# Kernel optimization log

Measured on AMD Instinct MI355X. Metric: run time of the kernel, lower is better.

Reference implementation:

```python
import jax, jax.numpy as jnp
import numpy as np

DIM = 512
NUM_HEADS = 16
HEAD_DIM = DIM // NUM_HEADS  # 32
SCALE = HEAD_DIM ** -0.5
B_, N = 1024, 49  # num_windows*batch, window_size**2


def setup_inputs() -> dict:
    key = jax.random.key(0)
    ks = jax.random.split(key, 12)
    s = DIM ** -0.5
    return {
        "x": jax.random.normal(ks[0], (B_, N, DIM), jnp.float32),
        "x2": jax.random.normal(ks[1], (B_, N, DIM), jnp.float32),
        "x3": jax.random.normal(ks[2], (B_, N, DIM), jnp.float32),
        # Linear weights stored as [in, out] (y = x @ W + b), same math as torch Linear
        "Wqkv": jax.random.normal(ks[3], (DIM, 3 * DIM), jnp.float32) * s,
        "bqkv": jnp.zeros((3 * DIM,), jnp.float32),
        "Wqkv2": jax.random.normal(ks[4], (DIM, 3 * DIM), jnp.float32) * s,
        "bqkv2": jnp.zeros((3 * DIM,), jnp.float32),
        "Wgw": jax.random.normal(ks[5], (DIM, DIM), jnp.float32) * s,
        "bgw": jnp.zeros((DIM,), jnp.float32),
        "Wproj": jax.random.normal(ks[6], (DIM, DIM), jnp.float32) * s,
        "bproj": jnp.zeros((DIM,), jnp.float32),
        "a": jnp.zeros((1,), jnp.float32),
    }


def reference(x, x2, x3, Wqkv, bqkv, Wqkv2, bqkv2, Wgw, bgw, Wproj, bproj, a):
    B, Nn, C = x.shape
    H, D = NUM_HEADS, HEAD_DIM
    # qkv from x: only k is actually used downstream
    qkv = (x @ Wqkv + bqkv).reshape(B, Nn, 3, H, D)
    k = jnp.transpose(qkv[:, :, 1], (0, 2, 1, 3))  # [B,H,N,D]
    # qkv2 from x3: q1 (gated query) and v1 (value + residual)
    qkv1 = (x3 @ Wqkv2 + bqkv2).reshape(B, Nn, 3, H, D)
    q1 = jnp.transpose(qkv1[:, :, 0], (0, 2, 1, 3))  # [B,H,N,D]
    v1 = jnp.transpose(qkv1[:, :, 2], (0, 2, 1, 3))  # [B,H,N,D]
    # gate from x2
    gw = jnp.transpose((x2 @ Wgw + bgw).reshape(B, Nn, H, D), (0, 2, 1, 3))
    q = q1 * SCALE * gw
    attn = jax.nn.softmax(jnp.einsum("bhnd,bhmd->bhnm", q, k), axis=-1)
    out = jnp.einsum("bhnm,bhmd->bhnd", attn, v1) + v1 * a
    out = jnp.transpose(out, (0, 2, 1, 3)).reshape(B, Nn, C)
    return out @ Wproj + bproj
```

## Files before the change

kernel.cpp:

```cpp
#include <hip/hip_runtime.h>

#define MR 50176
#define DIMC 512
#define NWIN 49
#define NBATCH 1024
#define NHEADS 16
#define ATTN_SCALE 0.17677669529663689f

typedef short bf16x8 __attribute__((ext_vector_type(8)));
typedef float f32x4 __attribute__((ext_vector_type(4)));
typedef unsigned int u32;

__device__ __forceinline__ unsigned short f2bf(float f) {
  union { float f; u32 u; } v; v.f = f;
  u32 u = v.u;
  u += 0x7FFFu + ((u >> 16) & 1u);
  return (unsigned short)(u >> 16);
}
__device__ __forceinline__ float bits_f(u32 u) {
  union { u32 u; float f; } v; v.u = u; return v.f;
}

__device__ __forceinline__ size_t pk_chunk(int r, int c) {
  return (((size_t)(r >> 3) * 8 + (c >> 3)) * 64 +
          ((r & 7) * 8 + ((c & 7) ^ (r & 7)))) << 4;
}

typedef const __attribute__((address_space(1))) u32* gp_t;
typedef __attribute__((address_space(3))) u32* lp_t;
__device__ __forceinline__ void glds16(const void* g, void* l) {
  __builtin_amdgcn_global_load_lds((gp_t)g, (lp_t)l, 16, 0, 0);
}

__global__ __launch_bounds__(256) void conv_pack3(
    const float* __restrict__ X0, const float* __restrict__ X1,
    const float* __restrict__ X2, short* __restrict__ P0,
    short* __restrict__ P1, short* __restrict__ P2) {
  const float* X = (blockIdx.y == 0) ? X0 : (blockIdx.y == 1) ? X1 : X2;
  short* Xp = (blockIdx.y == 0) ? P0 : (blockIdx.y == 1) ? P1 : P2;
  const int tid = blockIdx.x * 256 + threadIdx.x;
  const int li = tid & 63, gl = tid >> 6;
  const int kline = gl & 7, group = gl >> 3;
  const int rr = li >> 3, pp = li & 7;
  const int row = group * 8 + rr;
  const int k = kline * 64 + ((pp ^ rr) << 3);
  const float* src = X + (size_t)row * DIMC + k;
  const float4 a = *(const float4*)src;
  const float4 b = *(const float4*)(src + 4);
  u32 w0 = (u32)f2bf(a.x) | ((u32)f2bf(a.y) << 16);
  u32 w1 = (u32)f2bf(a.z) | ((u32)f2bf(a.w) << 16);
  u32 w2 = (u32)f2bf(b.x) | ((u32)f2bf(b.y) << 16);
  u32 w3 = (u32)f2bf(b.z) | ((u32)f2bf(b.w) << 16);
  ((uint4*)Xp)[tid] = make_uint4(w0, w1, w2, w3);
}

__global__ __launch_bounds__(256) void prep_w_pack(
    const float* __restrict__ Wqkv, const float* __restrict__ Wqkv2,
    const float* __restrict__ Wgw, const float* __restrict__ Wproj,
    short* __restrict__ Wp) {
  const int tid = blockIdx.x * 256 + threadIdx.x;
  const int li = tid & 63, gl = tid >> 6;
  const int kline = gl & 7, group = gl >> 3;
  const int rr = li >> 3, pp = li & 7;
  const int row = group * 8 + rr;
  const int k = kline * 64 + ((pp ^ rr) << 3);
  const int n = row & 511, mat = row >> 9;
  const float* W; int ldw, col;
  if (mat == 0)      { W = Wqkv;  ldw = 1536; col = 512 + n; }
  else if (mat == 1) { W = Wqkv2; ldw = 1536; col = n; }
  else if (mat == 2) { W = Wqkv2; ldw = 1536; col = 1024 + n; }
  else if (mat == 3) { W = Wgw;   ldw = 512;  col = n; }
  else               { W = Wproj; ldw = 512;  col = n; }
  unsigned short h[8];
#pragma unroll
  for (int j = 0; j < 8; ++j) h[j] = f2bf(W[(size_t)(k + j) * ldw + col]);
  u32 w0 = (u32)h[0] | ((u32)h[1] << 16);
  u32 w1 = (u32)h[2] | ((u32)h[3] << 16);
  u32 w2 = (u32)h[4] | ((u32)h[5] << 16);
  u32 w3 = (u32)h[6] | ((u32)h[7] << 16);
  ((uint4*)Wp)[tid] = make_uint4(w0, w1, w2, w3);
}

struct GemmCfg {
  const short* A[4];
  const float* bias[4];
  short* out[4];
  int wrow0[4];
};

template <int LNX, bool OUT_F32>
__global__ __launch_bounds__(256) void gemm_glds(
    GemmCfg cfg, const short* __restrict__ Wp, float* __restrict__ outf) {
  __shared__ short As[128 * 64];
  __shared__ short Bs[128 * 64];

  const int t = threadIdx.x, w = t >> 6, lane = t & 63;
  const int l15 = lane & 15, q = lane >> 4;
  const int wm = w >> 1, wn = w & 1;
  const int id = blockIdx.x;
  const int xcd = id & 7, slot = id >> 3;
  const int bx = slot & ((1 << LNX) - 1);
  const int y = xcd + ((slot >> LNX) << 3);
  const int row0 = y * 128;
  const int unit = bx >> 2, sub = bx & 3;
  const short* Ap = cfg.A[unit];
  const float* bias = cfg.bias[unit];
  short* outb = cfg.out[unit];
  const int nw0 = cfg.wrow0[unit] + sub * 128;
  const int col0 = sub * 128;

  f32x4 acc[4][4];
#pragma unroll
  for (int i = 0; i < 4; ++i)
#pragma unroll
    for (int j = 0; j < 4; ++j) acc[i][j] = {0.f, 0.f, 0.f, 0.f};

  const size_t lb = (size_t)lane * 16;
  const int r7 = l15 & 7, hi8 = l15 >> 3;

  for (int kt = 0; kt < 8; ++kt) {
    __syncthreads();
#pragma unroll
    for (int jj = 0; jj < 4; ++jj) {
      const int rg = w * 4 + jj;
      const char* ga = (const char*)Ap + ((((size_t)(row0 >> 3) + rg) * 8 + kt) << 10);
      glds16(ga + lb, &As[(size_t)rg << 9]);
      const char* gb = (const char*)Wp + ((((size_t)(nw0 >> 3) + rg) * 8 + kt) << 10);
      glds16(gb + lb, &Bs[(size_t)rg << 9]);
    }
    __syncthreads();
#pragma unroll
    for (int s = 0; s < 2; ++s) {
      const int sw = ((s * 4 + q) ^ r7);
      const int pos = (r7 * 8 + sw) * 8;
      bf16x8 af[4], bfr[4];
#pragma unroll
      for (int i = 0; i < 4; ++i)
        af[i] = *(const bf16x8*)&As[((wm * 8 + i * 2 + hi8) << 9) + pos];
#pragma unroll
      for (int j = 0; j < 4; ++j)
        bfr[j] = *(const bf16x8*)&Bs[((wn * 8 + j * 2 + hi8) << 9) + pos];
#pragma unroll
      for (int i = 0; i < 4; ++i)
#pragma unroll
        for (int j = 0; j < 4; ++j)
          acc[i][j] = __builtin_amdgcn_mfma_f32_16x16x32_bf16(af[i], bfr[j],
                                                              acc[i][j], 0, 0, 0);
    }
  }

#pragma unroll
  for (int j = 0; j < 4; ++j) {
    const int C = col0 + wn * 64 + j * 16 + l15;
    const float bv = bias[C];
#pragma unroll
    for (int i = 0; i < 4; ++i) {
#pragma unroll
      for (int r = 0; r < 4; ++r) {
        const int R = row0 + wm * 64 + i * 16 + q * 4 + r;
        const float val = acc[i][j][r] + bv;
        if constexpr (OUT_F32)
          outf[(size_t)R * DIMC + C] = val;
        else
          *(short*)((char*)outb + pk_chunk(R, C >> 3) + ((C & 7) << 1)) =
              (short)f2bf(val);
      }
    }
  }
}

__global__ __launch_bounds__(256) void attn_mfma(
    const short* __restrict__ kbuf, const short* __restrict__ qbuf,
    const short* __restrict__ vbuf, const short* __restrict__ gbuf,
    const float* __restrict__ a_scalar, short* __restrict__ obuf) {
  __shared__ short pls[4][64 * 40];
  __shared__ short vls[4][32 * 72];

  const int t = threadIdx.x;
  const int w = t >> 6, lane = t & 63;
  const int l15 = lane & 15, q = lane >> 4;
  const int wid = blockIdx.x * 4 + w;
  const int b = wid >> 4, h = wid & 15;
  const int row0 = b * NWIN;
  const float aval = a_scalar[0];
  short* P = pls[w];
  short* VT = vls[w];

#pragma unroll
  for (int it = 0; it < 5; ++it) {
    int off = (it * 64 + lane) * 8;
    if (off < 32 * 72) *(uint4*)&VT[off] = make_uint4(0u, 0u, 0u, 0u);
  }

  bf16x8 kf[4];
#pragma unroll
  for (int mj = 0; mj < 4; ++mj) {
    int m = mj * 16 + l15; if (m > 48) m = 48;
    kf[mj] = *(const bf16x8*)((const char*)kbuf + pk_chunk(row0 + m, h * 4 + q));
  }
  bf16x8 qf[4];
#pragma unroll
  for (int mi = 0; mi < 4; ++mi) {
    int n = mi * 16 + l15; if (n > 48) n = 48;
    const size_t off = pk_chunk(row0 + n, h * 4 + q);
    uint4 qa = *(const uint4*)((const char*)qbuf + off);
    uint4 ga = *(const uint4*)((const char*)gbuf + off);
    u32* qa_ = (u32*)&qa;
    u32* ga_ = (u32*)&ga;
    uint4 res; u32* r_ = (u32*)&res;
#pragma unroll
    for (int jj = 0; jj < 4; ++jj) {
      float lo = bits_f(qa_[jj] << 16) * bits_f(ga_[jj] << 16);
      float hi = bits_f(qa_[jj] & 0xffff0000u) * bits_f(ga_[jj] & 0xffff0000u);
      r_[jj] = (u32)f2bf(lo) | ((u32)f2bf(hi) << 16);
    }
    qf[mi] = *(bf16x8*)&res;
  }
#pragma unroll
  for (int it = 0; it < 4; ++it) {
    int chunk = it * 64 + lane;
    if (chunk < 196) {
      int n = chunk >> 2, dcq = chunk & 3;
      uint4 v = *(const uint4*)((const char*)vbuf + pk_chunk(row0 + n, h * 4 + dcq));
      const short* vs = (const short*)&v;
#pragma unroll
      for (int j = 0; j < 8; ++j) VT[(dcq * 8 + j) * 72 + n] = vs[j];
    }
  }

  f32x4 s[4][4];
#pragma unroll
  for (int mi = 0; mi < 4; ++mi)
#pragma unroll
    for (int nj = 0; nj < 4; ++nj) {
      f32x4 z = {0.f, 0.f, 0.f, 0.f};
      s[mi][nj] = __builtin_amdgcn_mfma_f32_16x16x32_bf16(qf[mi], kf[nj], z, 0, 0, 0);
    }

#pragma unroll
  for (int mi = 0; mi < 4; ++mi)
#pragma unroll
    for (int nj = 0; nj < 4; ++nj) {
      const bool valid = (nj * 16 + l15) < NWIN;
#pragma unroll
      for (int r = 0; r < 4; ++r)
        s[mi][nj][r] = valid ? __expf(ATTN_SCALE * s[mi][nj][r]) : 0.f;
    }

  float lsum[4][4];
#pragma unroll
  for (int mi = 0; mi < 4; ++mi)
#pragma unroll
    for (int r = 0; r < 4; ++r) {
      float part = s[mi][0][r] + s[mi][1][r] + s[mi][2][r] + s[mi][3][r];
      part += __shfl_xor(part, 1, 64);
      part += __shfl_xor(part, 2, 64);
      part += __shfl_xor(part, 4, 64);
      part += __shfl_xor(part, 8, 64);
      lsum[mi][r] = part;
    }

  f32x4 o[4][2];
#pragma unroll
  for (int mi = 0; mi < 4; ++mi)
#pragma unroll
    for (int dj = 0; dj < 2; ++dj) o[mi][dj] = {0.f, 0.f, 0.f, 0.f};

#pragma unroll
  for (int c = 0; c < 2; ++c) {
#pragma unroll
    for (int mi = 0; mi < 4; ++mi)
#pragma unroll
      for (int njh = 0; njh < 2; ++njh) {
        const int nj = c * 2 + njh;
        const int m = nj * 16 + l15;
#pragma unroll
        for (int r = 0; r < 4; ++r) {
          const int n = mi * 16 + q * 4 + r;
          float val = s[mi][nj][r];
          if (m == n) val += aval * lsum[mi][r];
          P[n * 40 + njh * 16 + l15] = (short)f2bf(val);
        }
      }
    bf16x8 bfr[2];
#pragma unroll
    for (int dj = 0; dj < 2; ++dj)
      bfr[dj] = *(const bf16x8*)&VT[(dj * 16 + l15) * 72 + c * 32 + q * 8];
#pragma unroll
    for (int mi = 0; mi < 4; ++mi) {
      bf16x8 af = *(const bf16x8*)&P[(mi * 16 + l15) * 40 + q * 8];
#pragma unroll
      for (int dj = 0; dj < 2; ++dj)
        o[mi][dj] = __builtin_amdgcn_mfma_f32_16x16x32_bf16(af, bfr[dj],
                                                            o[mi][dj], 0, 0, 0);
    }
  }

#pragma unroll
  for (int mi = 0; mi < 4; ++mi)
#pragma unroll
    for (int r = 0; r < 4; ++r) {
      const int n = mi * 16 + q * 4 + r;
      if (n < NWIN) {
        const float rl = 1.0f / lsum[mi][r];
#pragma unroll
        for (int dj = 0; dj < 2; ++dj) {
          const int d = dj * 16 + l15;
          *(short*)((char*)obuf + pk_chunk(row0 + n, h * 4 + (d >> 3)) +
                    ((d & 7) << 1)) = (short)f2bf(o[mi][dj][r] * rl);
        }
      }
    }
}

extern "C" void kernel_launch(void* const* d_in, const int* in_sizes, int n_in,
                              void* d_out, int out_size, void* d_ws,
                              size_t ws_size, hipStream_t stream) {
  const float* x     = (const float*)d_in[0];
  const float* x2    = (const float*)d_in[1];
  const float* x3    = (const float*)d_in[2];
  const float* Wqkv  = (const float*)d_in[3];
  const float* bqkv  = (const float*)d_in[4];
  const float* Wqkv2 = (const float*)d_in[5];
  const float* bqkv2 = (const float*)d_in[6];
  const float* Wgw   = (const float*)d_in[7];
  const float* bgw   = (const float*)d_in[8];
  const float* Wproj = (const float*)d_in[9];
  const float* bproj = (const float*)d_in[10];
  const float* a     = (const float*)d_in[11];

  char* ws = (char*)d_ws;
  const size_t WTSZ = (size_t)2560 * DIMC * sizeof(short);
  const size_t BSZ  = (size_t)MR * DIMC * sizeof(short);
  short* wt_all = (short*)ws;

  prep_w_pack<<<640, 256, 0, stream>>>(Wqkv, Wqkv2, Wgw, Wproj, wt_all);

  const int convg = MR * DIMC / 8 / 256;

  if (ws_size >= WTSZ + 7 * BSZ) {
    short* xp   = (short*)(ws + WTSZ);
    short* x2p  = (short*)(ws + WTSZ + BSZ);
    short* x3p  = (short*)(ws + WTSZ + 2 * BSZ);
    short* kbuf = (short*)(ws + WTSZ + 3 * BSZ);
    short* qbuf = (short*)(ws + WTSZ + 4 * BSZ);
    short* vbuf = (short*)(ws + WTSZ + 5 * BSZ);
    short* gbuf = (short*)(ws + WTSZ + 6 * BSZ);
    short* obuf = xp;

    conv_pack3<<<dim3(convg, 3), 256, 0, stream>>>(x, x2, x3, xp, x2p, x3p);

    GemmCfg s1;
    s1.A[0] = xp;  s1.A[1] = x3p; s1.A[2] = x3p; s1.A[3] = x2p;
    s1.bias[0] = bqkv + 512; s1.bias[1] = bqkv2;
    s1.bias[2] = bqkv2 + 1024; s1.bias[3] = bgw;
    s1.out[0] = kbuf; s1.out[1] = qbuf; s1.out[2] = vbuf; s1.out[3] = gbuf;
    s1.wrow0[0] = 0; s1.wrow0[1] = 512; s1.wrow0[2] = 1024; s1.wrow0[3] = 1536;
    gemm_glds<4, false><<<16 * 392, 256, 0, stream>>>(s1, wt_all, nullptr);

    attn_mfma<<<(NBATCH * NHEADS) / 4, 256, 0, stream>>>(kbuf, qbuf, vbuf,
                                                         gbuf, a, obuf);

    GemmCfg pj = {};
    pj.A[0] = obuf; pj.bias[0] = bproj; pj.out[0] = nullptr; pj.wrow0[0] = 2048;
    gemm_glds<2, true><<<4 * 392, 256, 0, stream>>>(pj, wt_all, (float*)d_out);
  } else {
    short* cb   = (short*)(ws + WTSZ);
    short* kbuf = (short*)(ws + WTSZ + BSZ);
    short* qbuf = (short*)(ws + WTSZ + 2 * BSZ);
    short* vbuf = (short*)(ws + WTSZ + 3 * BSZ);
    short* gbuf = (short*)(ws + WTSZ + 4 * BSZ);
    short* obuf = cb;

    conv_pack3<<<dim3(convg, 1), 256, 0, stream>>>(x, x, x, cb, cb, cb);
    GemmCfg ck = {};
    ck.A[0] = cb; ck.bias[0] = bqkv + 512; ck.out[0] = kbuf; ck.wrow0[0] = 0;
    gemm_glds<2, false><<<4 * 392, 256, 0, stream>>>(ck, wt_all, nullptr);

    conv_pack3<<<dim3(convg, 1), 256, 0, stream>>>(x3, x3, x3, cb, cb, cb);
    GemmCfg cqv = {};
    cqv.A[0] = cb; cqv.A[1] = cb;
    cqv.bias[0] = bqkv2; cqv.bias[1] = bqkv2 + 1024;
    cqv.out[0] = qbuf; cqv.out[1] = vbuf;
    cqv.wrow0[0] = 512; cqv.wrow0[1] = 1024;
    gemm_glds<3, false><<<8 * 392, 256, 0, stream>>>(cqv, wt_all, nullptr);

    conv_pack3<<<dim3(convg, 1), 256, 0, stream>>>(x2, x2, x2, cb, cb, cb);
    GemmCfg cg = {};
    cg.A[0] = cb; cg.bias[0] = bgw; cg.out[0] = gbuf; cg.wrow0[0] = 1536;
    gemm_glds<2, false><<<4 * 392, 256, 0, stream>>>(cg, wt_all, nullptr);

    attn_mfma<<<(NBATCH * NHEADS) / 4, 256, 0, stream>>>(kbuf, qbuf, vbuf,
                                                         gbuf, a, obuf);

    GemmCfg pj = {};
    pj.A[0] = obuf; pj.bias[0] = bproj; pj.wrow0[0] = 2048;
    gemm_glds<2, true><<<4 * 392, 256, 0, stream>>>(pj, wt_all, (float*)d_out);
  }
}
```

Before: 624.4 us.

## Replace GEMM with 256x256-tile, 8-wave, double-buffered pipelined kernel

```diff
diff --git a/kernel.cpp b/kernel.cpp
--- a/kernel.cpp
+++ b/kernel.cpp
@@ -88,81 +88,175 @@
   int wrow0[4];
 };
 
-template <int LNX, bool OUT_F32>
-__global__ __launch_bounds__(256) void gemm_glds(
+template <int LBX, bool OUT_F32>
+__global__ __launch_bounds__(512, 2) void gemm8p(
     GemmCfg cfg, const short* __restrict__ Wp, float* __restrict__ outf) {
-  __shared__ short As[128 * 64];
-  __shared__ short Bs[128 * 64];
+  __shared__ short As[2][16384];
+  __shared__ short Bs[2][16384];
 
   const int t = threadIdx.x, w = t >> 6, lane = t & 63;
   const int l15 = lane & 15, q = lane >> 4;
-  const int wm = w >> 1, wn = w & 1;
+  const int wm = w >> 2, wn = w & 3;
+  const int r7 = l15 & 7, hi8 = l15 >> 3;
+
   const int id = blockIdx.x;
-  const int xcd = id & 7, slot = id >> 3;
-  const int bx = slot & ((1 << LNX) - 1);
-  const int y = xcd + ((slot >> LNX) << 3);
-  const int row0 = y * 128;
-  const int unit = bx >> 2, sub = bx & 3;
+  const int spx = gridDim.x >> 3;
+  const int flat = (id & 7) * spx + (id >> 3);
+  const int bx = flat & ((1 << LBX) - 1);
+  const int mtile = flat >> LBX;
+  const int unit = bx >> 1, sub = bx & 1;
+  const int row0 = mtile * 256;
+  const int col0 = sub * 256;
   const short* Ap = cfg.A[unit];
   const float* bias = cfg.bias[unit];
   short* outb = cfg.out[unit];
-  const int nw0 = cfg.wrow0[unit] + sub * 128;
-  const int col0 = sub * 128;
-
-  f32x4 acc[4][4];
-#pragma unroll
-  for (int i = 0; i < 4; ++i)
+  const int nw0 = cfg.wrow0[unit] + sub * 256;
+
+  const int in0 = (r7 * 8 + (q ^ r7)) << 4;
+  const int in1 = (r7 * 8 + ((4 + q) ^ r7)) << 4;
+
+  auto stage = [&](int pt, int c) {
+    if (c >= 8) return;
+    const int slot = c & 1;
+#pragma unroll
+    for (int jj = 0; jj < 2; ++jj) {
+      const int cb = w * 2 + jj;
+      if (pt < 2) {
+        const int rowblk = ((cb & 8) ? 16 : 0) + pt * 8 + (cb & 7);
+        const char* ga = (const char*)Ap +
+            ((((size_t)(row0 >> 3) + rowblk) * 8 + c) << 10) +
+            (size_t)lane * 16;
+        glds16(ga, (char*)&As[slot][0] + (((pt << 4) + cb) << 10));
+      } else {
+        const int p = pt - 2;
+        const int colblk = ((cb >> 2) << 3) + p * 4 + (cb & 3);
+        const char* gb = (const char*)Wp +
+            ((((size_t)(nw0 >> 3) + colblk) * 8 + c) << 10) +
+            (size_t)lane * 16;
+        glds16(gb, (char*)&Bs[slot][0] + (((p << 4) + cb) << 10));
+      }
+    }
+  };
+
+  f32x4 acc[8][4];
+#pragma unroll
+  for (int i = 0; i < 8; ++i)
 #pragma unroll
     for (int j = 0; j < 4; ++j) acc[i][j] = {0.f, 0.f, 0.f, 0.f};
 
-  const size_t lb = (size_t)lane * 16;
-  const int r7 = l15 & 7, hi8 = l15 >> 3;
-
-  for (int kt = 0; kt < 8; ++kt) {
-    __syncthreads();
-#pragma unroll
-    for (int jj = 0; jj < 4; ++jj) {
-      const int rg = w * 4 + jj;
-      const char* ga = (const char*)Ap + ((((size_t)(row0 >> 3) + rg) * 8 + kt) << 10);
-      glds16(ga + lb, &As[(size_t)rg << 9]);
-      const char* gb = (const char*)Wp + ((((size_t)(nw0 >> 3) + rg) * 8 + kt) << 10);
-      glds16(gb + lb, &Bs[(size_t)rg << 9]);
-    }
-    __syncthreads();
-#pragma unroll
-    for (int s = 0; s < 2; ++s) {
-      const int sw = ((s * 4 + q) ^ r7);
-      const int pos = (r7 * 8 + sw) * 8;
-      bf16x8 af[4], bfr[4];
-#pragma unroll
-      for (int i = 0; i < 4; ++i)
-        af[i] = *(const bf16x8*)&As[((wm * 8 + i * 2 + hi8) << 9) + pos];
-#pragma unroll
-      for (int j = 0; j < 4; ++j)
-        bfr[j] = *(const bf16x8*)&Bs[((wn * 8 + j * 2 + hi8) << 9) + pos];
-#pragma unroll
-      for (int i = 0; i < 4; ++i)
-#pragma unroll
-        for (int j = 0; j < 4; ++j)
-          acc[i][j] = __builtin_amdgcn_mfma_f32_16x16x32_bf16(af[i], bfr[j],
-                                                              acc[i][j], 0, 0, 0);
-    }
-  }
-
-#pragma unroll
-  for (int j = 0; j < 4; ++j) {
-    const int C = col0 + wn * 64 + j * 16 + l15;
+  stage(0, 0); stage(3, 0); stage(1, 0); stage(2, 0);
+  stage(0, 1); stage(3, 1);
+  asm volatile("s_waitcnt vmcnt(4)" ::: "memory");
+  asm volatile("s_barrier" ::: "memory");
+
+  for (int c = 0; c < 8; ++c) {
+    const char* Ab = (const char*)&As[c & 1][0];
+    const char* Bb = (const char*)&Bs[c & 1][0];
+    bf16x8 af[4][2], bfA[2][2], bfB[2][2];
+
+#pragma unroll
+    for (int i = 0; i < 4; ++i) {
+      const int o = (wm * 8 + i * 2 + hi8) << 10;
+      af[i][0] = *(const bf16x8*)(Ab + o + in0);
+      af[i][1] = *(const bf16x8*)(Ab + o + in1);
+    }
+#pragma unroll
+    for (int j = 0; j < 2; ++j) {
+      const int o = (wn * 4 + j * 2 + hi8) << 10;
+      bfA[j][0] = *(const bf16x8*)(Bb + o + in0);
+      bfA[j][1] = *(const bf16x8*)(Bb + o + in1);
+    }
+    stage(1, c + 1);
+    asm volatile("s_barrier" ::: "memory");
+    __builtin_amdgcn_s_setprio(1);
+#pragma unroll
+    for (int i = 0; i < 4; ++i)
+#pragma unroll
+      for (int j = 0; j < 2; ++j) {
+        acc[i][j] = __builtin_amdgcn_mfma_f32_16x16x32_bf16(
+            af[i][0], bfA[j][0], acc[i][j], 0, 0, 0);
+        acc[i][j] = __builtin_amdgcn_mfma_f32_16x16x32_bf16(
+            af[i][1], bfA[j][1], acc[i][j], 0, 0, 0);
+      }
+    __builtin_amdgcn_s_setprio(0);
+    asm volatile("s_barrier" ::: "memory");
+
+#pragma unroll
+    for (int j = 0; j < 2; ++j) {
+      const int o = (16 + wn * 4 + j * 2 + hi8) << 10;
+      bfB[j][0] = *(const bf16x8*)(Bb + o + in0);
+      bfB[j][1] = *(const bf16x8*)(Bb + o + in1);
+    }
+    stage(2, c + 1);
+    asm volatile("s_barrier" ::: "memory");
+    __builtin_amdgcn_s_setprio(1);
+#pragma unroll
+    for (int i = 0; i < 4; ++i)
+#pragma unroll
+      for (int j = 0; j < 2; ++j) {
+        acc[i][2 + j] = __builtin_amdgcn_mfma_f32_16x16x32_bf16(
+            af[i][0], bfB[j][0], acc[i][2 + j], 0, 0, 0);
+        acc[i][2 + j] = __builtin_amdgcn_mfma_f32_16x16x32_bf16(
+            af[i][1], bfB[j][1], acc[i][2 + j], 0, 0, 0);
+      }
+    __builtin_amdgcn_s_setprio(0);
+    asm volatile("s_barrier" ::: "memory");
+
+#pragma unroll
+    for (int i = 0; i < 4; ++i) {
+      const int o = (16 + wm * 8 + i * 2 + hi8) << 10;
+      af[i][0] = *(const bf16x8*)(Ab + o + in0);
+      af[i][1] = *(const bf16x8*)(Ab + o + in1);
+    }
+    stage(0, c + 2);
+    asm volatile("s_barrier" ::: "memory");
+    __builtin_amdgcn_s_setprio(1);
+#pragma unroll
+    for (int i = 0; i < 4; ++i)
+#pragma unroll
+      for (int j = 0; j < 2; ++j) {
+        acc[4 + i][2 + j] = __builtin_amdgcn_mfma_f32_16x16x32_bf16(
+            af[i][0], bfB[j][0], acc[4 + i][2 + j], 0, 0, 0);
+        acc[4 + i][2 + j] = __builtin_amdgcn_mfma_f32_16x16x32_bf16(
+            af[i][1], bfB[j][1], acc[4 + i][2 + j], 0, 0, 0);
+      }
+    __builtin_amdgcn_s_setprio(0);
+    asm volatile("s_barrier" ::: "memory");
+
+    stage(3, c + 2);
+    asm volatile("s_barrier" ::: "memory");
+    __builtin_amdgcn_s_setprio(1);
+#pragma unroll
+    for (int i = 0; i < 4; ++i)
+#pragma unroll
+      for (int j = 0; j < 2; ++j) {
+        acc[4 + i][j] = __builtin_amdgcn_mfma_f32_16x16x32_bf16(
+            af[i][0], bfA[j][0], acc[4 + i][j], 0, 0, 0);
+        acc[4 + i][j] = __builtin_amdgcn_mfma_f32_16x16x32_bf16(
+            af[i][1], bfA[j][1], acc[4 + i][j], 0, 0, 0);
+      }
+    __builtin_amdgcn_s_setprio(0);
+    if (c < 6)
+      asm volatile("s_waitcnt vmcnt(4)" ::: "memory");
+    else
+      asm volatile("s_waitcnt vmcnt(0)" ::: "memory");
+    asm volatile("s_barrier" ::: "memory");
+  }
+
+#pragma unroll
+  for (int ci = 0; ci < 4; ++ci) {
+    const int C = col0 + wn * 64 + (ci >> 1) * 32 + (ci & 1) * 16 + l15;
     const float bv = bias[C];
 #pragma unroll
-    for (int i = 0; i < 4; ++i) {
+    for (int ri = 0; ri < 8; ++ri) {
+      const int R = row0 + wm * 128 + (ri >> 2) * 64 + (ri & 3) * 16 + q * 4;
 #pragma unroll
       for (int r = 0; r < 4; ++r) {
-        const int R = row0 + wm * 64 + i * 16 + q * 4 + r;
-        const float val = acc[i][j][r] + bv;
+        const float val = acc[ri][ci][r] + bv;
         if constexpr (OUT_F32)
-          outf[(size_t)R * DIMC + C] = val;
+          outf[(size_t)(R + r) * DIMC + C] = val;
         else
-          *(short*)((char*)outb + pk_chunk(R, C >> 3) + ((C & 7) << 1)) =
+          *(short*)((char*)outb + pk_chunk(R + r, C >> 3) + ((C & 7) << 1)) =
               (short)f2bf(val);
       }
     }
@@ -356,14 +450,14 @@
     s1.bias[2] = bqkv2 + 1024; s1.bias[3] = bgw;
     s1.out[0] = kbuf; s1.out[1] = qbuf; s1.out[2] = vbuf; s1.out[3] = gbuf;
     s1.wrow0[0] = 0; s1.wrow0[1] = 512; s1.wrow0[2] = 1024; s1.wrow0[3] = 1536;
-    gemm_glds<4, false><<<16 * 392, 256, 0, stream>>>(s1, wt_all, nullptr);
+    gemm8p<3, false><<<1568, 512, 0, stream>>>(s1, wt_all, nullptr);
 
     attn_mfma<<<(NBATCH * NHEADS) / 4, 256, 0, stream>>>(kbuf, qbuf, vbuf,
                                                          gbuf, a, obuf);
 
     GemmCfg pj = {};
     pj.A[0] = obuf; pj.bias[0] = bproj; pj.out[0] = nullptr; pj.wrow0[0] = 2048;
-    gemm_glds<2, true><<<4 * 392, 256, 0, stream>>>(pj, wt_all, (float*)d_out);
+    gemm8p<1, true><<<392, 512, 0, stream>>>(pj, wt_all, (float*)d_out);
   } else {
     short* cb   = (short*)(ws + WTSZ);
     short* kbuf = (short*)(ws + WTSZ + BSZ);
@@ -375,7 +469,7 @@
     conv_pack3<<<dim3(convg, 1), 256, 0, stream>>>(x, x, x, cb, cb, cb);
     GemmCfg ck = {};
     ck.A[0] = cb; ck.bias[0] = bqkv + 512; ck.out[0] = kbuf; ck.wrow0[0] = 0;
-    gemm_glds<2, false><<<4 * 392, 256, 0, stream>>>(ck, wt_all, nullptr);
+    gemm8p<1, false><<<392, 512, 0, stream>>>(ck, wt_all, nullptr);
 
     conv_pack3<<<dim3(convg, 1), 256, 0, stream>>>(x3, x3, x3, cb, cb, cb);
     GemmCfg cqv = {};
@@ -383,18 +477,18 @@
     cqv.bias[0] = bqkv2; cqv.bias[1] = bqkv2 + 1024;
     cqv.out[0] = qbuf; cqv.out[1] = vbuf;
     cqv.wrow0[0] = 512; cqv.wrow0[1] = 1024;
-    gemm_glds<3, false><<<8 * 392, 256, 0, stream>>>(cqv, wt_all, nullptr);
+    gemm8p<2, false><<<784, 512, 0, stream>>>(cqv, wt_all, nullptr);
 
     conv_pack3<<<dim3(convg, 1), 256, 0, stream>>>(x2, x2, x2, cb, cb, cb);
     GemmCfg cg = {};
     cg.A[0] = cb; cg.bias[0] = bgw; cg.out[0] = gbuf; cg.wrow0[0] = 1536;
-    gemm_glds<2, false><<<4 * 392, 256, 0, stream>>>(cg, wt_all, nullptr);
+    gemm8p<1, false><<<392, 512, 0, stream>>>(cg, wt_all, nullptr);
 
     attn_mfma<<<(NBATCH * NHEADS) / 4, 256, 0, stream>>>(kbuf, qbuf, vbuf,
                                                          gbuf, a, obuf);
 
     GemmCfg pj = {};
     pj.A[0] = obuf; pj.bias[0] = bproj; pj.wrow0[0] = 2048;
-    gemm_glds<2, true><<<4 * 392, 256, 0, stream>>>(pj, wt_all, (float*)d_out);
-  }
-}
+    gemm8p<1, true><<<392, 512, 0, stream>>>(pj, wt_all, (float*)d_out);
+  }
+}
```

Result: no change. 629.3 us (+0.8%).

## Fuse fp32-to-bf16 input conversion into QKV GEMM A-tile loading

Applied to the files above, without the earlier changes.

```diff
diff --git a/kernel.cpp b/kernel.cpp
--- a/kernel.cpp
+++ b/kernel.cpp
@@ -30,28 +30,6 @@
 typedef __attribute__((address_space(3))) u32* lp_t;
 __device__ __forceinline__ void glds16(const void* g, void* l) {
   __builtin_amdgcn_global_load_lds((gp_t)g, (lp_t)l, 16, 0, 0);
-}
-
-__global__ __launch_bounds__(256) void conv_pack3(
-    const float* __restrict__ X0, const float* __restrict__ X1,
-    const float* __restrict__ X2, short* __restrict__ P0,
-    short* __restrict__ P1, short* __restrict__ P2) {
-  const float* X = (blockIdx.y == 0) ? X0 : (blockIdx.y == 1) ? X1 : X2;
-  short* Xp = (blockIdx.y == 0) ? P0 : (blockIdx.y == 1) ? P1 : P2;
-  const int tid = blockIdx.x * 256 + threadIdx.x;
-  const int li = tid & 63, gl = tid >> 6;
-  const int kline = gl & 7, group = gl >> 3;
-  const int rr = li >> 3, pp = li & 7;
-  const int row = group * 8 + rr;
-  const int k = kline * 64 + ((pp ^ rr) << 3);
-  const float* src = X + (size_t)row * DIMC + k;
-  const float4 a = *(const float4*)src;
-  const float4 b = *(const float4*)(src + 4);
-  u32 w0 = (u32)f2bf(a.x) | ((u32)f2bf(a.y) << 16);
-  u32 w1 = (u32)f2bf(a.z) | ((u32)f2bf(a.w) << 16);
-  u32 w2 = (u32)f2bf(b.x) | ((u32)f2bf(b.y) << 16);
-  u32 w3 = (u32)f2bf(b.z) | ((u32)f2bf(b.w) << 16);
-  ((uint4*)Xp)[tid] = make_uint4(w0, w1, w2, w3);
 }
 
 __global__ __launch_bounds__(256) void prep_w_pack(
@@ -83,12 +61,13 @@
 
 struct GemmCfg {
   const short* A[4];
+  const float* Af[4];
   const float* bias[4];
   short* out[4];
   int wrow0[4];
 };
 
-template <int LNX, bool OUT_F32>
+template <int LNX, bool OUT_F32, bool CONVA>
 __global__ __launch_bounds__(256) void gemm_glds(
     GemmCfg cfg, const short* __restrict__ Wp, float* __restrict__ outf) {
   __shared__ short As[128 * 64];
@@ -103,7 +82,6 @@
   const int y = xcd + ((slot >> LNX) << 3);
   const int row0 = y * 128;
   const int unit = bx >> 2, sub = bx & 3;
-  const short* Ap = cfg.A[unit];
   const float* bias = cfg.bias[unit];
   short* outb = cfg.out[unit];
   const int nw0 = cfg.wrow0[unit] + sub * 128;
@@ -118,34 +96,100 @@
   const size_t lb = (size_t)lane * 16;
   const int r7 = l15 & 7, hi8 = l15 >> 3;
 
-  for (int kt = 0; kt < 8; ++kt) {
-    __syncthreads();
+  if constexpr (CONVA) {
+    const int rr = lane >> 3, pp = lane & 7;
+    const float* abase =
+        cfg.Af[unit] + (size_t)(row0 + w * 32 + rr) * DIMC + ((pp ^ rr) << 3);
+    float4 ar[4][2];
 #pragma unroll
     for (int jj = 0; jj < 4; ++jj) {
-      const int rg = w * 4 + jj;
-      const char* ga = (const char*)Ap + ((((size_t)(row0 >> 3) + rg) * 8 + kt) << 10);
-      glds16(ga + lb, &As[(size_t)rg << 9]);
-      const char* gb = (const char*)Wp + ((((size_t)(nw0 >> 3) + rg) * 8 + kt) << 10);
-      glds16(gb + lb, &Bs[(size_t)rg << 9]);
-    }
-    __syncthreads();
-#pragma unroll
-    for (int s = 0; s < 2; ++s) {
-      const int sw = ((s * 4 + q) ^ r7);
-      const int pos = (r7 * 8 + sw) * 8;
-      bf16x8 af[4], bfr[4];
-#pragma unroll
-      for (int i = 0; i < 4; ++i)
-        af[i] = *(const bf16x8*)&As[((wm * 8 + i * 2 + hi8) << 9) + pos];
-#pragma unroll
-      for (int j = 0; j < 4; ++j)
-        bfr[j] = *(const bf16x8*)&Bs[((wn * 8 + j * 2 + hi8) << 9) + pos];
-#pragma unroll
-      for (int i = 0; i < 4; ++i)
+      const float* s = abase + (size_t)jj * 8 * DIMC;
+      ar[jj][0] = *(const float4*)s;
+      ar[jj][1] = *(const float4*)(s + 4);
+    }
+    for (int kt = 0; kt < 8; ++kt) {
+      asm volatile("s_barrier" ::: "memory");
+#pragma unroll
+      for (int jj = 0; jj < 4; ++jj) {
+        const int rg = w * 4 + jj;
+        const char* gb =
+            (const char*)Wp + ((((size_t)(nw0 >> 3) + rg) * 8 + kt) << 10);
+        glds16(gb + lb, &Bs[(size_t)rg << 9]);
+      }
+      asm volatile("s_waitcnt vmcnt(4)" ::: "memory");
+#pragma unroll
+      for (int jj = 0; jj < 4; ++jj) {
+        u32 w0 = (u32)f2bf(ar[jj][0].x) | ((u32)f2bf(ar[jj][0].y) << 16);
+        u32 w1 = (u32)f2bf(ar[jj][0].z) | ((u32)f2bf(ar[jj][0].w) << 16);
+        u32 w2 = (u32)f2bf(ar[jj][1].x) | ((u32)f2bf(ar[jj][1].y) << 16);
+        u32 w3 = (u32)f2bf(ar[jj][1].z) | ((u32)f2bf(ar[jj][1].w) << 16);
+        *(uint4*)&As[(((size_t)(w * 4 + jj)) << 9) + (size_t)lane * 8] =
+            make_uint4(w0, w1, w2, w3);
+      }
+      if (kt < 7) {
+#pragma unroll
+        for (int jj = 0; jj < 4; ++jj) {
+          const float* s = abase + (size_t)jj * 8 * DIMC + (kt + 1) * 64;
+          ar[jj][0] = *(const float4*)s;
+          ar[jj][1] = *(const float4*)(s + 4);
+        }
+        asm volatile("s_waitcnt vmcnt(8) lgkmcnt(0)" ::: "memory");
+      } else {
+        asm volatile("s_waitcnt vmcnt(0) lgkmcnt(0)" ::: "memory");
+      }
+      asm volatile("s_barrier" ::: "memory");
+#pragma unroll
+      for (int s = 0; s < 2; ++s) {
+        const int sw = ((s * 4 + q) ^ r7);
+        const int pos = (r7 * 8 + sw) * 8;
+        bf16x8 af[4], bfr[4];
+#pragma unroll
+        for (int i = 0; i < 4; ++i)
+          af[i] = *(const bf16x8*)&As[((wm * 8 + i * 2 + hi8) << 9) + pos];
 #pragma unroll
         for (int j = 0; j < 4; ++j)
-          acc[i][j] = __builtin_amdgcn_mfma_f32_16x16x32_bf16(af[i], bfr[j],
-                                                              acc[i][j], 0, 0, 0);
+          bfr[j] = *(const bf16x8*)&Bs[((wn * 8 + j * 2 + hi8) << 9) + pos];
+#pragma unroll
+        for (int i = 0; i < 4; ++i)
+#pragma unroll
+          for (int j = 0; j < 4; ++j)
+            acc[i][j] = __builtin_amdgcn_mfma_f32_16x16x32_bf16(
+                af[i], bfr[j], acc[i][j], 0, 0, 0);
+      }
+    }
+  } else {
+    const short* Ap = cfg.A[unit];
+    for (int kt = 0; kt < 8; ++kt) {
+      __syncthreads();
+#pragma unroll
+      for (int jj = 0; jj < 4; ++jj) {
+        const int rg = w * 4 + jj;
+        const char* ga =
+            (const char*)Ap + ((((size_t)(row0 >> 3) + rg) * 8 + kt) << 10);
+        glds16(ga + lb, &As[(size_t)rg << 9]);
+        const char* gb =
+            (const char*)Wp + ((((size_t)(nw0 >> 3) + rg) * 8 + kt) << 10);
+        glds16(gb + lb, &Bs[(size_t)rg << 9]);
+      }
+      __syncthreads();
+#pragma unroll
+      for (int s = 0; s < 2; ++s) {
+        const int sw = ((s * 4 + q) ^ r7);
+        const int pos = (r7 * 8 + sw) * 8;
+        bf16x8 af[4], bfr[4];
+#pragma unroll
+        for (int i = 0; i < 4; ++i)
+          af[i] = *(const bf16x8*)&As[((wm * 8 + i * 2 + hi8) << 9) + pos];
+#pragma unroll
+        for (int j = 0; j < 4; ++j)
+          bfr[j] = *(const bf16x8*)&Bs[((wn * 8 + j * 2 + hi8) << 9) + pos];
+#pragma unroll
+        for (int i = 0; i < 4; ++i)
+#pragma unroll
+          for (int j = 0; j < 4; ++j)
+            acc[i][j] = __builtin_amdgcn_mfma_f32_16x16x32_bf16(
+                af[i], bfr[j], acc[i][j], 0, 0, 0);
+      }
     }
   }
 
@@ -334,67 +378,27 @@
   const size_t BSZ  = (size_t)MR * DIMC * sizeof(short);
   short* wt_all = (short*)ws;
 
+  short* kbuf = (short*)(ws + WTSZ);
+  short* qbuf = (short*)(ws + WTSZ + BSZ);
+  short* vbuf = (short*)(ws + WTSZ + 2 * BSZ);
+  short* gbuf = (short*)(ws + WTSZ + 3 * BSZ);
+  short* obuf = (short*)(ws + WTSZ + 4 * BSZ);
+
   prep_w_pack<<<640, 256, 0, stream>>>(Wqkv, Wqkv2, Wgw, Wproj, wt_all);
 
-  const int convg = MR * DIMC / 8 / 256;
-
-  if (ws_size >= WTSZ + 7 * BSZ) {
-    short* xp   = (short*)(ws + WTSZ);
-    short* x2p  = (short*)(ws + WTSZ + BSZ);
-    short* x3p  = (short*)(ws + WTSZ + 2 * BSZ);
-    short* kbuf = (short*)(ws + WTSZ + 3 * BSZ);
-    short* qbuf = (short*)(ws + WTSZ + 4 * BSZ);
-    short* vbuf = (short*)(ws + WTSZ + 5 * BSZ);
-    short* gbuf = (short*)(ws + WTSZ + 6 * BSZ);
-    short* obuf = xp;
-
-    conv_pack3<<<dim3(convg, 3), 256, 0, stream>>>(x, x2, x3, xp, x2p, x3p);
-
-    GemmCfg s1;
-    s1.A[0] = xp;  s1.A[1] = x3p; s1.A[2] = x3p; s1.A[3] = x2p;
-    s1.bias[0] = bqkv + 512; s1.bias[1] = bqkv2;
-    s1.bias[2] = bqkv2 + 1024; s1.bias[3] = bgw;
-    s1.out[0] = kbuf; s1.out[1] = qbuf; s1.out[2] = vbuf; s1.out[3] = gbuf;
-    s1.wrow0[0] = 0; s1.wrow0[1] = 512; s1.wrow0[2] = 1024; s1.wrow0[3] = 1536;
-    gemm_glds<4, false><<<16 * 392, 256, 0, stream>>>(s1, wt_all, nullptr);
-
-    attn_mfma<<<(NBATCH * NHEADS) / 4, 256, 0, stream>>>(kbuf, qbuf, vbuf,
-                                                         gbuf, a, obuf);
-
-    GemmCfg pj = {};
-    pj.A[0] = obuf; pj.bias[0] = bproj; pj.out[0] = nullptr; pj.wrow0[0] = 2048;
-    gemm_glds<2, true><<<4 * 392, 256, 0, stream>>>(pj, wt_all, (float*)d_out);
-  } else {
-    short* cb   = (short*)(ws + WTSZ);
-    short* kbuf = (short*)(ws + WTSZ + BSZ);
-    short* qbuf = (short*)(ws + WTSZ + 2 * BSZ);
-    short* vbuf = (short*)(ws + WTSZ + 3 * BSZ);
-    short* gbuf = (short*)(ws + WTSZ + 4 * BSZ);
-    short* obuf = cb;
-
-    conv_pack3<<<dim3(convg, 1), 256, 0, stream>>>(x, x, x, cb, cb, cb);
-    GemmCfg ck = {};
-    ck.A[0] = cb; ck.bias[0] = bqkv + 512; ck.out[0] = kbuf; ck.wrow0[0] = 0;
-    gemm_glds<2, false><<<4 * 392, 256, 0, stream>>>(ck, wt_all, nullptr);
-
-    conv_pack3<<<dim3(convg, 1), 256, 0, stream>>>(x3, x3, x3, cb, cb, cb);
-    GemmCfg cqv = {};
-    cqv.A[0] = cb; cqv.A[1] = cb;
-    cqv.bias[0] = bqkv2; cqv.bias[1] = bqkv2 + 1024;
-    cqv.out[0] = qbuf; cqv.out[1] = vbuf;
-    cqv.wrow0[0] = 512; cqv.wrow0[1] = 1024;
-    gemm_glds<3, false><<<8 * 392, 256, 0, stream>>>(cqv, wt_all, nullptr);
-
-    conv_pack3<<<dim3(convg, 1), 256, 0, stream>>>(x2, x2, x2, cb, cb, cb);
-    GemmCfg cg = {};
-    cg.A[0] = cb; cg.bias[0] = bgw; cg.out[0] = gbuf; cg.wrow0[0] = 1536;
-    gemm_glds<2, false><<<4 * 392, 256, 0, stream>>>(cg, wt_all, nullptr);
-
-    attn_mfma<<<(NBATCH * NHEADS) / 4, 256, 0, stream>>>(kbuf, qbuf, vbuf,
-                                                         gbuf, a, obuf);
-
-    GemmCfg pj = {};
-    pj.A[0] = obuf; pj.bias[0] = bproj; pj.wrow0[0] = 2048;
-    gemm_glds<2, true><<<4 * 392, 256, 0, stream>>>(pj, wt_all, (float*)d_out);
-  }
-}
+  GemmCfg s1 = {};
+  s1.Af[0] = x;  s1.Af[1] = x3; s1.Af[2] = x3; s1.Af[3] = x2;
+  s1.bias[0] = bqkv + 512; s1.bias[1] = bqkv2;
+  s1.bias[2] = bqkv2 + 1024; s1.bias[3] = bgw;
+  s1.out[0] = kbuf; s1.out[1] = qbuf; s1.out[2] = vbuf; s1.out[3] = gbuf;
+  s1.wrow0[0] = 0; s1.wrow0[1] = 512; s1.wrow0[2] = 1024; s1.wrow0[3] = 1536;
+  gemm_glds<4, false, true><<<16 * 392, 256, 0, stream>>>(s1, wt_all, nullptr);
+
+  attn_mfma<<<(NBATCH * NHEADS) / 4, 256, 0, stream>>>(kbuf, qbuf, vbuf,
+                                                       gbuf, a, obuf);
+
+  GemmCfg pj = {};
+  pj.A[0] = obuf; pj.bias[0] = bproj; pj.out[0] = nullptr; pj.wrow0[0] = 2048;
+  gemm_glds<2, true, false><<<4 * 392, 256, 0, stream>>>(pj, wt_all,
+                                                         (float*)d_out);
+}
```

Result: no change. 612.7 us (-1.9%).
